# Kernel tuning notes

Measured on AMD Instinct MI355X. Metric: run time of the kernel, lower is better.

## Reference

```python
import jax, jax.numpy as jnp
import numpy as np

HIDDEN = 256
HEADS = 8
DK = HIDDEN // HEADS
BH = 16  # bias_h_size
N = 2048
B = 1


def setup_inputs() -> dict:
    key = jax.random.key(0)
    ks = jax.random.split(key, 20)
    s = 0.02
    inp = {
        "int_chain_label": jax.random.randint(ks[0], (N, N), 0, 2, dtype=jnp.int32),
        "dist_map": jax.random.uniform(ks[1], (N, N), dtype=jnp.float32),
        "contact_map": jax.random.uniform(ks[2], (N, N), dtype=jnp.float32),
        "q": jax.random.normal(ks[3], (B, N, HIDDEN), dtype=jnp.float32),
        "k": jax.random.normal(ks[4], (B, N, HIDDEN), dtype=jnp.float32),
        "v": jax.random.normal(ks[5], (B, N, HIDDEN), dtype=jnp.float32),
        # projections
        "Wq": jax.random.normal(ks[6], (HIDDEN, HIDDEN), dtype=jnp.float32) * s,
        "bq": jnp.zeros((HIDDEN,), jnp.float32),
        "Wk": jax.random.normal(ks[7], (HIDDEN, HIDDEN), dtype=jnp.float32) * s,
        "bk": jnp.zeros((HIDDEN,), jnp.float32),
        "Wv": jax.random.normal(ks[8], (HIDDEN, HIDDEN), dtype=jnp.float32) * s,
        "bv": jnp.zeros((HIDDEN,), jnp.float32),
        "Wo": jax.random.normal(ks[9], (HIDDEN, HIDDEN), dtype=jnp.float32) * s,
        "bo": jnp.zeros((HIDDEN,), jnp.float32),
        # distance bias MLP: Linear(2, BH) -> Linear(BH, 1)
        "Wd1": jax.random.normal(ks[10], (2, BH), dtype=jnp.float32) * 0.5,
        "bd1": jnp.zeros((BH,), jnp.float32),
        "Wd2": jax.random.normal(ks[11], (BH, 1), dtype=jnp.float32) * 0.5,
        "bd2": jnp.zeros((1,), jnp.float32),
        # contact bias MLP
        "Wc1": jax.random.normal(ks[12], (2, BH), dtype=jnp.float32) * 0.5,
        "bc1": jnp.zeros((BH,), jnp.float32),
        "Wc2": jax.random.normal(ks[13], (BH, 1), dtype=jnp.float32) * 0.5,
        "bc2": jnp.zeros((1,), jnp.float32),
    }
    return inp


def _pair_bias(mp, label_f, W1, b1, W2, b2):
    # stack(map, label) -> [N,N,2]; two linears (no nonlinearity in original) -> [N,N]
    x = jnp.stack((mp, label_f), axis=-1)
    h = x @ W1 + b1                      # [N,N,BH]
    return (h @ W2 + b2)[..., 0]          # [N,N]


def reference(int_chain_label, dist_map, contact_map, q, k, v,
              Wq, bq, Wk, bk, Wv, bv, Wo, bo,
              Wd1, bd1, Wd2, bd2, Wc1, bc1, Wc2, bc2):
    label_f = int_chain_label.astype(jnp.float32)
    bias = (_pair_bias(dist_map, label_f, Wd1, bd1, Wd2, bd2)
            + _pair_bias(contact_map, label_f, Wc1, bc1, Wc2, bc2))  # [N,N]
    bias = bias[None, None]  # [1,1,N,N] broadcast over batch, heads

    b, n, _ = q.shape
    scale = DK ** -0.5
    qh = (q @ Wq + bq).reshape(b, n, HEADS, DK).transpose(0, 2, 1, 3) * scale  # [B,H,N,D]
    kh = (k @ Wk + bk).reshape(b, n, HEADS, DK).transpose(0, 2, 1, 3)
    vh = (v @ Wv + bv).reshape(b, n, HEADS, DK).transpose(0, 2, 1, 3)

    scores = jnp.einsum('bhnd,bhmd->bhnm', qh, kh) + bias  # [B,H,N,N]
    attn = jax.nn.softmax(scores, axis=-1)
    out = jnp.einsum('bhnm,bhmd->bhnd', attn, vh)           # [B,H,N,D]
    out = out.transpose(0, 2, 1, 3).reshape(b, n, HEADS * DK)
    return out @ Wo + bo
```

## Files before the change

kernel.cpp:

```cpp
#include <hip/hip_runtime.h>
#include <hip/hip_bf16.h>

#define SN 2048
#define HD 256
#define NHEAD 8
#define DK 32
#define BH 16
#define KCH 4
#define KTILES 8

typedef __bf16 bf16;
typedef __bf16 bf16x8 __attribute__((ext_vector_type(8)));
typedef __bf16 bf16x4 __attribute__((ext_vector_type(4)));
typedef float f32x4 __attribute__((ext_vector_type(4)));
typedef int i32x4 __attribute__((ext_vector_type(4)));

__global__ void __launch_bounds__(256) prep_wt_kernel(
    const float* __restrict__ Wq, const float* __restrict__ Wk,
    const float* __restrict__ Wv, const float* __restrict__ Wo,
    bf16* __restrict__ wt)
{
    __shared__ bf16 tile[32][HD + 8];
    int mat = blockIdx.x >> 3, rc = blockIdx.x & 7;
    int t = threadIdx.x;
    const float* W = mat == 0 ? Wq : mat == 1 ? Wk : mat == 2 ? Wv : Wo;
    bf16* Wt = wt + mat * HD * HD;
    int r0 = rc * 32;
    #pragma unroll
    for (int i = 0; i < 32; i++) tile[i][t] = (bf16)W[(r0 + i) * HD + t];
    __syncthreads();
    #pragma unroll
    for (int i = 0; i < 32; i++) Wt[t * HD + r0 + i] = tile[i][t];
}

template<bool AF32, int MODE, bool OUTF32>
__device__ __forceinline__ void gemm_body(
    const void* __restrict__ Ap, const bf16* __restrict__ Wt,
    const float* __restrict__ bias, void* __restrict__ outp, int bid)
{
    int wave = threadIdx.x >> 6, lane = threadIdx.x & 63;
    int g = lane >> 4, qi = lane & 15;
    int mblk = bid & 31, nblk = bid >> 5;
    int m0 = mblk * 64 + wave * 16, n0 = nblk * 32;
    f32x4 acc0 = {0.f, 0.f, 0.f, 0.f}, acc1 = {0.f, 0.f, 0.f, 0.f};
    const bf16* W0 = Wt + (n0 + qi) * HD + 8 * g;
    const bf16* W1 = W0 + 16 * HD;
    #pragma unroll
    for (int ks = 0; ks < 8; ks++) {
        bf16x8 a;
        if constexpr (AF32) {
            const float* Ar = (const float*)Ap + (m0 + qi) * HD + 8 * g + ks * 32;
            f32x4 lo = *(const f32x4*)Ar;
            f32x4 hi = *(const f32x4*)(Ar + 4);
            #pragma unroll
            for (int e = 0; e < 4; e++) { a[e] = (bf16)lo[e]; a[4 + e] = (bf16)hi[e]; }
        } else {
            a = *(const bf16x8*)((const bf16*)Ap + (m0 + qi) * HD + 8 * g + ks * 32);
        }
        bf16x8 b0 = *(const bf16x8*)(W0 + ks * 32);
        bf16x8 b1 = *(const bf16x8*)(W1 + ks * 32);
        acc0 = __builtin_amdgcn_mfma_f32_16x16x32_bf16(a, b0, acc0, 0, 0, 0);
        acc1 = __builtin_amdgcn_mfma_f32_16x16x32_bf16(a, b1, acc1, 0, 0, 0);
    }
    float bv0 = bias[n0 + qi], bv1 = bias[n0 + 16 + qi];
    if constexpr (MODE == 0) {
        if constexpr (OUTF32) {
            float* out = (float*)outp;
            #pragma unroll
            for (int r = 0; r < 4; r++) {
                int m = m0 + 4 * g + r;
                out[m * HD + n0 + qi]      = acc0[r] + bv0;
                out[m * HD + n0 + 16 + qi] = acc1[r] + bv1;
            }
        } else {
            bf16* out = (bf16*)outp;
            #pragma unroll
            for (int r = 0; r < 4; r++) {
                int m = m0 + 4 * g + r;
                out[m * HD + n0 + qi]      = (bf16)(acc0[r] + bv0);
                out[m * HD + n0 + 16 + qi] = (bf16)(acc1[r] + bv1);
            }
        }
    } else {
        bf16* out = (bf16*)outp;
        bf16x4 v0, v1;
        #pragma unroll
        for (int r = 0; r < 4; r++) { v0[r] = (bf16)(acc0[r] + bv0); v1[r] = (bf16)(acc1[r] + bv1); }
        *(bf16x4*)(out + (n0 + qi) * SN + m0 + 4 * g)      = v0;
        *(bf16x4*)(out + (n0 + 16 + qi) * SN + m0 + 4 * g) = v1;
    }
}

__global__ void __launch_bounds__(256) qkv_kernel(
    const float* __restrict__ q, const float* __restrict__ k, const float* __restrict__ v,
    const bf16* __restrict__ wt,
    const float* __restrict__ bq, const float* __restrict__ bk, const float* __restrict__ bv,
    bf16* __restrict__ qh, bf16* __restrict__ kh, bf16* __restrict__ vt)
{
    int w = blockIdx.y;
    if (w == 0)      gemm_body<true, 0, false>(q, wt,               bq, qh, blockIdx.x);
    else if (w == 1) gemm_body<true, 0, false>(k, wt + HD * HD,     bk, kh, blockIdx.x);
    else             gemm_body<true, 1, false>(v, wt + 2 * HD * HD, bv, vt, blockIdx.x);
}

__global__ void __launch_bounds__(256) oproj_kernel(
    const bf16* __restrict__ A, const bf16* __restrict__ wt3,
    const float* __restrict__ bo, float* __restrict__ out)
{
    gemm_body<false, 0, true>(A, wt3, bo, out, blockIdx.x);
}

__global__ void __launch_bounds__(128) attn_kernel(
    const bf16* __restrict__ qh, const bf16* __restrict__ kh,
    const bf16* __restrict__ vt,
    const int* __restrict__ label, const float* __restrict__ dist,
    const float* __restrict__ contact,
    const float* __restrict__ Wd1, const float* __restrict__ bd1,
    const float* __restrict__ Wd2, const float* __restrict__ bd2,
    const float* __restrict__ Wc1, const float* __restrict__ bc1,
    const float* __restrict__ Wc2, const float* __restrict__ bc2,
    float* __restrict__ po, float* __restrict__ pm, float* __restrict__ pl)
{
    int wave = threadIdx.x >> 6, lane = threadIdx.x & 63;
    int g = lane >> 4, qi = lane & 15;
    int h = blockIdx.x >> 8, qb = (blockIdx.x >> 2) & 63, c = blockIdx.x & 3;
    int q0 = qb * 32 + wave * 16;
    int kbase = c * (KTILES * 64);

    float ad = 0.f, bld = 0.f, dd = bd2[0];
    #pragma unroll
    for (int j = 0; j < BH; j++) {
        float w2 = Wd2[j];
        ad  += Wd1[j] * w2;
        bld += Wd1[BH + j] * w2;
        dd  += bd1[j] * w2;
    }
    float ac = 0.f, blc = 0.f, dc = bc2[0];
    #pragma unroll
    for (int j = 0; j < BH; j++) {
        float w2 = Wc2[j];
        ac  += Wc1[j] * w2;
        blc += Wc1[BH + j] * w2;
        dc  += bc1[j] * w2;
    }
    float bl = bld + blc, dl = dd + dc;

    __shared__ bf16 plds[2][16][72];
    bf16 (*P)[72] = plds[wave];

    bf16x8 qf = *(const bf16x8*)(qh + (q0 + qi) * HD + h * DK + 8 * g);
    const bf16* kp  = kh + h * DK + 8 * g + kbase * HD;
    const bf16* v0p = vt + (h * DK + qi) * SN + 8 * g + kbase;
    const bf16* v1p = v0p + 16 * SN;
    const float* dp = dist    + (q0 + qi) * SN + 4 * g + kbase;
    const float* cp = contact + (q0 + qi) * SN + 4 * g + kbase;
    const int*   lp = label   + (q0 + qi) * SN + 4 * g + kbase;

    const float scale = 0.17677669529663687f;
    float m = -1e30f, lsum = 0.f;
    f32x4 o0 = {0.f, 0.f, 0.f, 0.f}, o1 = {0.f, 0.f, 0.f, 0.f};

    for (int kt = 0; kt < KTILES; kt++) {
        int key0 = kt * 64;
        bf16x8 kf0 = *(const bf16x8*)(kp + (key0 +  0 + qi) * HD);
        bf16x8 kf1 = *(const bf16x8*)(kp + (key0 + 16 + qi) * HD);
        bf16x8 kf2 = *(const bf16x8*)(kp + (key0 + 32 + qi) * HD);
        bf16x8 kf3 = *(const bf16x8*)(kp + (key0 + 48 + qi) * HD);
        f32x4 dv0 = *(const f32x4*)(dp + key0 +  0), dv1 = *(const f32x4*)(dp + key0 + 16);
        f32x4 dv2 = *(const f32x4*)(dp + key0 + 32), dv3 = *(const f32x4*)(dp + key0 + 48);
        f32x4 cv0 = *(const f32x4*)(cp + key0 +  0), cv1 = *(const f32x4*)(cp + key0 + 16);
        f32x4 cv2 = *(const f32x4*)(cp + key0 + 32), cv3 = *(const f32x4*)(cp + key0 + 48);
        i32x4 lv0 = *(const i32x4*)(lp + key0 +  0), lv1 = *(const i32x4*)(lp + key0 + 16);
        i32x4 lv2 = *(const i32x4*)(lp + key0 + 32), lv3 = *(const i32x4*)(lp + key0 + 48);
        f32x4 zero = {0.f, 0.f, 0.f, 0.f};
        f32x4 s0 = __builtin_amdgcn_mfma_f32_16x16x32_bf16(kf0, qf, zero, 0, 0, 0);
        f32x4 s1 = __builtin_amdgcn_mfma_f32_16x16x32_bf16(kf1, qf, zero, 0, 0, 0);
        f32x4 s2 = __builtin_amdgcn_mfma_f32_16x16x32_bf16(kf2, qf, zero, 0, 0, 0);
        f32x4 s3 = __builtin_amdgcn_mfma_f32_16x16x32_bf16(kf3, qf, zero, 0, 0, 0);
        float x[16];
        #pragma unroll
        for (int r = 0; r < 4; r++) {
            float b0 = ad * dv0[r] + ac * cv0[r] + bl * (float)lv0[r] + dl;
            float b1 = ad * dv1[r] + ac * cv1[r] + bl * (float)lv1[r] + dl;
            float b2 = ad * dv2[r] + ac * cv2[r] + bl * (float)lv2[r] + dl;
            float b3 = ad * dv3[r] + ac * cv3[r] + bl * (float)lv3[r] + dl;
            x[r]      = s0[r] * scale + b0;
            x[4 + r]  = s1[r] * scale + b1;
            x[8 + r]  = s2[r] * scale + b2;
            x[12 + r] = s3[r] * scale + b3;
        }
        float t0 = fmaxf(x[0], x[1]),  t1 = fmaxf(x[2], x[3]);
        float t2 = fmaxf(x[4], x[5]),  t3 = fmaxf(x[6], x[7]);
        float t4 = fmaxf(x[8], x[9]),  t5 = fmaxf(x[10], x[11]);
        float t6 = fmaxf(x[12], x[13]), t7 = fmaxf(x[14], x[15]);
        float tm = fmaxf(fmaxf(fmaxf(t0, t1), fmaxf(t2, t3)),
                         fmaxf(fmaxf(t4, t5), fmaxf(t6, t7)));
        tm = fmaxf(tm, __shfl_xor(tm, 16));
        tm = fmaxf(tm, __shfl_xor(tm, 32));
        float mnew = fmaxf(m, tm);
        float f = __expf(m - mnew);
        float ps = 0.f;
        #pragma unroll
        for (int i = 0; i < 16; i++) { x[i] = __expf(x[i] - mnew); ps += x[i]; }
        ps += __shfl_xor(ps, 16);
        ps += __shfl_xor(ps, 32);
        lsum = lsum * f + ps;
        m = mnew;
        #pragma unroll
        for (int r = 0; r < 4; r++) { o0[r] *= f; o1[r] *= f; }
        #pragma unroll
        for (int s = 0; s < 4; s++) {
            bf16x4 pv;
            #pragma unroll
            for (int r = 0; r < 4; r++) pv[r] = (bf16)x[s * 4 + r];
            *(bf16x4*)(&P[qi][16 * s + 4 * g]) = pv;
        }
        asm volatile("" ::: "memory");
        bf16x4 pa0 = *(const bf16x4*)(&P[qi][8 * g]);
        bf16x4 pa1 = *(const bf16x4*)(&P[qi][8 * g + 4]);
        bf16x4 pa2 = *(const bf16x4*)(&P[qi][32 + 8 * g]);
        bf16x4 pa3 = *(const bf16x4*)(&P[qi][32 + 8 * g + 4]);
        asm volatile("" ::: "memory");
        bf16x8 pb0 = __builtin_shufflevector(pa0, pa1, 0, 1, 2, 3, 4, 5, 6, 7);
        bf16x8 pb1 = __builtin_shufflevector(pa2, pa3, 0, 1, 2, 3, 4, 5, 6, 7);
        bf16x8 va00 = *(const bf16x8*)(v0p + key0);
        bf16x8 va01 = *(const bf16x8*)(v0p + key0 + 32);
        bf16x8 va10 = *(const bf16x8*)(v1p + key0);
        bf16x8 va11 = *(const bf16x8*)(v1p + key0 + 32);
        o0 = __builtin_amdgcn_mfma_f32_16x16x32_bf16(va00, pb0, o0, 0, 0, 0);
        o0 = __builtin_amdgcn_mfma_f32_16x16x32_bf16(va01, pb1, o0, 0, 0, 0);
        o1 = __builtin_amdgcn_mfma_f32_16x16x32_bf16(va10, pb0, o1, 0, 0, 0);
        o1 = __builtin_amdgcn_mfma_f32_16x16x32_bf16(va11, pb1, o1, 0, 0, 0);
    }
    int hq = h * SN + q0 + qi;
    *(f32x4*)(po + (hq * KCH + c) * DK + 4 * g)      = o0;
    *(f32x4*)(po + (hq * KCH + c) * DK + 16 + 4 * g) = o1;
    if (g == 0) { pm[hq * KCH + c] = m; pl[hq * KCH + c] = lsum; }
}

__global__ void __launch_bounds__(256) combine_kernel(
    const float* __restrict__ po, const float* __restrict__ pm,
    const float* __restrict__ pl, bf16* __restrict__ aout)
{
    int idx = blockIdx.x * 256 + threadIdx.x;
    int d = idx & (DK - 1), hq = idx >> 5;
    int h = hq >> 11, qr = hq & (SN - 1);
    f32x4 mv = *(const f32x4*)(pm + hq * KCH);
    f32x4 lv = *(const f32x4*)(pl + hq * KCH);
    float M = fmaxf(fmaxf(mv[0], mv[1]), fmaxf(mv[2], mv[3]));
    float w0 = __expf(mv[0] - M), w1 = __expf(mv[1] - M);
    float w2 = __expf(mv[2] - M), w3 = __expf(mv[3] - M);
    float L = w0 * lv[0] + w1 * lv[1] + w2 * lv[2] + w3 * lv[3];
    const float* p = po + hq * KCH * DK + d;
    float o = w0 * p[0] + w1 * p[DK] + w2 * p[2 * DK] + w3 * p[3 * DK];
    aout[qr * HD + h * DK + d] = (bf16)(o / L);
}

extern "C" void kernel_launch(void* const* d_in, const int* in_sizes, int n_in,
                              void* d_out, int out_size, void* d_ws, size_t ws_size,
                              hipStream_t stream)
{
    static const int expect[22] = {
        SN * SN, SN * SN, SN * SN,
        SN * HD, SN * HD, SN * HD,
        HD * HD, HD, HD * HD, HD,
        HD * HD, HD, HD * HD, HD,
        2 * BH, BH, BH, 1,
        2 * BH, BH, BH, 1
    };
    if (n_in != 22) return;
    for (int i = 0; i < 22; i++) if (in_sizes[i] != expect[i]) return;

    const int*   label   = (const int*)  d_in[0];
    const float* dist    = (const float*)d_in[1];
    const float* contact = (const float*)d_in[2];
    const float* q  = (const float*)d_in[3];
    const float* k  = (const float*)d_in[4];
    const float* v  = (const float*)d_in[5];
    const float* Wq = (const float*)d_in[6];  const float* bq = (const float*)d_in[7];
    const float* Wk = (const float*)d_in[8];  const float* bk = (const float*)d_in[9];
    const float* Wv = (const float*)d_in[10]; const float* bv = (const float*)d_in[11];
    const float* Wo = (const float*)d_in[12]; const float* bo = (const float*)d_in[13];
    const float* Wd1 = (const float*)d_in[14]; const float* bd1 = (const float*)d_in[15];
    const float* Wd2 = (const float*)d_in[16]; const float* bd2 = (const float*)d_in[17];
    const float* Wc1 = (const float*)d_in[18]; const float* bc1 = (const float*)d_in[19];
    const float* Wc2 = (const float*)d_in[20]; const float* bc2 = (const float*)d_in[21];

    char* ws = (char*)d_ws;
    bf16*  qh   = (bf16*)(ws);
    bf16*  kh   = (bf16*)(ws + (1u << 20));
    bf16*  vt   = (bf16*)(ws + (2u << 20));
    bf16*  aout = (bf16*)(ws + (3u << 20));
    bf16*  wt   = (bf16*)(ws + (4u << 20));
    float* po   = (float*)(ws + (5u << 20));
    float* pm   = (float*)(ws + (13u << 20));
    float* pl   = (float*)(ws + (13u << 20) + (256u << 10));

    prep_wt_kernel<<<dim3(32), 256, 0, stream>>>(Wq, Wk, Wv, Wo, wt);

    qkv_kernel<<<dim3(256, 3), 256, 0, stream>>>(q, k, v, wt, bq, bk, bv, qh, kh, vt);

    attn_kernel<<<dim3(NHEAD * 64 * KCH), 128, 0, stream>>>(
        qh, kh, vt, label, dist, contact,
        Wd1, bd1, Wd2, bd2, Wc1, bc1, Wc2, bc2, po, pm, pl);

    combine_kernel<<<dim3(NHEAD * SN * DK / 256), 256, 0, stream>>>(po, pm, pl, aout);

    oproj_kernel<<<dim3(256), 256, 0, stream>>>(aout, wt + 3 * HD * HD, bo, (float*)d_out);
}
```

Before: 221.2 us.

## Split attention keys eight ways, use shuffles for P, prefetch GEMM operands

Measured after the change: 222.7 us. No clear change (+0.7%).

```diff
diff --git a/kernel.cpp b/kernel.cpp
--- a/kernel.cpp
+++ b/kernel.cpp
@@ -6,14 +6,13 @@
 #define NHEAD 8
 #define DK 32
 #define BH 16
-#define KCH 4
-#define KTILES 8
 
 typedef __bf16 bf16;
 typedef __bf16 bf16x8 __attribute__((ext_vector_type(8)));
 typedef __bf16 bf16x4 __attribute__((ext_vector_type(4)));
 typedef float f32x4 __attribute__((ext_vector_type(4)));
 typedef int i32x4 __attribute__((ext_vector_type(4)));
+typedef unsigned uint4v __attribute__((ext_vector_type(4)));
 
 __global__ void __launch_bounds__(256) prep_wt_kernel(
     const float* __restrict__ Wq, const float* __restrict__ Wk,
@@ -45,22 +44,35 @@
     f32x4 acc0 = {0.f, 0.f, 0.f, 0.f}, acc1 = {0.f, 0.f, 0.f, 0.f};
     const bf16* W0 = Wt + (n0 + qi) * HD + 8 * g;
     const bf16* W1 = W0 + 16 * HD;
-    #pragma unroll
-    for (int ks = 0; ks < 8; ks++) {
-        bf16x8 a;
+
+    auto loadA = [&](int ks) -> bf16x8 {
         if constexpr (AF32) {
             const float* Ar = (const float*)Ap + (m0 + qi) * HD + 8 * g + ks * 32;
             f32x4 lo = *(const f32x4*)Ar;
             f32x4 hi = *(const f32x4*)(Ar + 4);
+            bf16x8 a;
             #pragma unroll
             for (int e = 0; e < 4; e++) { a[e] = (bf16)lo[e]; a[4 + e] = (bf16)hi[e]; }
+            return a;
         } else {
-            a = *(const bf16x8*)((const bf16*)Ap + (m0 + qi) * HD + 8 * g + ks * 32);
+            return *(const bf16x8*)((const bf16*)Ap + (m0 + qi) * HD + 8 * g + ks * 32);
         }
-        bf16x8 b0 = *(const bf16x8*)(W0 + ks * 32);
-        bf16x8 b1 = *(const bf16x8*)(W1 + ks * 32);
-        acc0 = __builtin_amdgcn_mfma_f32_16x16x32_bf16(a, b0, acc0, 0, 0, 0);
-        acc1 = __builtin_amdgcn_mfma_f32_16x16x32_bf16(a, b1, acc1, 0, 0, 0);
+    };
+
+    bf16x8 a_c  = loadA(0);
+    bf16x8 b0_c = *(const bf16x8*)(W0);
+    bf16x8 b1_c = *(const bf16x8*)(W1);
+    #pragma unroll
+    for (int ks = 0; ks < 8; ks++) {
+        bf16x8 a_n, b0_n, b1_n;
+        if (ks < 7) {
+            a_n  = loadA(ks + 1);
+            b0_n = *(const bf16x8*)(W0 + (ks + 1) * 32);
+            b1_n = *(const bf16x8*)(W1 + (ks + 1) * 32);
+        }
+        acc0 = __builtin_amdgcn_mfma_f32_16x16x32_bf16(a_c, b0_c, acc0, 0, 0, 0);
+        acc1 = __builtin_amdgcn_mfma_f32_16x16x32_bf16(a_c, b1_c, acc1, 0, 0, 0);
+        if (ks < 7) { a_c = a_n; b0_c = b0_n; b1_c = b1_n; }
     }
     float bv0 = bias[n0 + qi], bv1 = bias[n0 + 16 + qi];
     if constexpr (MODE == 0) {
@@ -110,6 +122,7 @@
     gemm_body<false, 0, true>(A, wt3, bo, out, blockIdx.x);
 }
 
+template<int KCHT>
 __global__ void __launch_bounds__(128) attn_kernel(
     const bf16* __restrict__ qh, const bf16* __restrict__ kh,
     const bf16* __restrict__ vt,
@@ -121,11 +134,14 @@
     const float* __restrict__ Wc2, const float* __restrict__ bc2,
     float* __restrict__ po, float* __restrict__ pm, float* __restrict__ pl)
 {
+    constexpr int KT = SN / KCHT / 64;
     int wave = threadIdx.x >> 6, lane = threadIdx.x & 63;
     int g = lane >> 4, qi = lane & 15;
-    int h = blockIdx.x >> 8, qb = (blockIdx.x >> 2) & 63, c = blockIdx.x & 3;
+    int h = blockIdx.x / (64 * KCHT);
+    int rem = blockIdx.x % (64 * KCHT);
+    int qb = rem / KCHT, c = rem % KCHT;
     int q0 = qb * 32 + wave * 16;
-    int kbase = c * (KTILES * 64);
+    int kbase = c * (KT * 64);
 
     float ad = 0.f, bld = 0.f, dd = bd2[0];
     #pragma unroll
@@ -144,9 +160,6 @@
         dc  += bc1[j] * w2;
     }
     float bl = bld + blc, dl = dd + dc;
-
-    __shared__ bf16 plds[2][16][72];
-    bf16 (*P)[72] = plds[wave];
 
     bf16x8 qf = *(const bf16x8*)(qh + (q0 + qi) * HD + h * DK + 8 * g);
     const bf16* kp  = kh + h * DK + 8 * g + kbase * HD;
@@ -160,7 +173,12 @@
     float m = -1e30f, lsum = 0.f;
     f32x4 o0 = {0.f, 0.f, 0.f, 0.f}, o1 = {0.f, 0.f, 0.f, 0.f};
 
-    for (int kt = 0; kt < KTILES; kt++) {
+    int src0 = ((lane >> 4) & 1) * 32 + (lane & 15);
+    int src1 = src0 + 16;
+    bool hi = lane >= 32;
+
+    #pragma unroll
+    for (int kt = 0; kt < KT; kt++) {
         int key0 = kt * 64;
         bf16x8 kf0 = *(const bf16x8*)(kp + (key0 +  0 + qi) * HD);
         bf16x8 kf1 = *(const bf16x8*)(kp + (key0 + 16 + qi) * HD);
@@ -172,6 +190,11 @@
         f32x4 cv2 = *(const f32x4*)(cp + key0 + 32), cv3 = *(const f32x4*)(cp + key0 + 48);
         i32x4 lv0 = *(const i32x4*)(lp + key0 +  0), lv1 = *(const i32x4*)(lp + key0 + 16);
         i32x4 lv2 = *(const i32x4*)(lp + key0 + 32), lv3 = *(const i32x4*)(lp + key0 + 48);
+        bf16x8 va00 = *(const bf16x8*)(v0p + key0);
+        bf16x8 va01 = *(const bf16x8*)(v0p + key0 + 32);
+        bf16x8 va10 = *(const bf16x8*)(v1p + key0);
+        bf16x8 va11 = *(const bf16x8*)(v1p + key0 + 32);
+
         f32x4 zero = {0.f, 0.f, 0.f, 0.f};
         f32x4 s0 = __builtin_amdgcn_mfma_f32_16x16x32_bf16(kf0, qf, zero, 0, 0, 0);
         f32x4 s1 = __builtin_amdgcn_mfma_f32_16x16x32_bf16(kf1, qf, zero, 0, 0, 0);
@@ -189,9 +212,9 @@
             x[8 + r]  = s2[r] * scale + b2;
             x[12 + r] = s3[r] * scale + b3;
         }
-        float t0 = fmaxf(x[0], x[1]),  t1 = fmaxf(x[2], x[3]);
-        float t2 = fmaxf(x[4], x[5]),  t3 = fmaxf(x[6], x[7]);
-        float t4 = fmaxf(x[8], x[9]),  t5 = fmaxf(x[10], x[11]);
+        float t0 = fmaxf(x[0], x[1]),   t1 = fmaxf(x[2], x[3]);
+        float t2 = fmaxf(x[4], x[5]),   t3 = fmaxf(x[6], x[7]);
+        float t4 = fmaxf(x[8], x[9]),   t5 = fmaxf(x[10], x[11]);
         float t6 = fmaxf(x[12], x[13]), t7 = fmaxf(x[14], x[15]);
         float tm = fmaxf(fmaxf(fmaxf(t0, t1), fmaxf(t2, t3)),
                          fmaxf(fmaxf(t4, t5), fmaxf(t6, t7)));
@@ -208,36 +231,42 @@
         m = mnew;
         #pragma unroll
         for (int r = 0; r < 4; r++) { o0[r] *= f; o1[r] *= f; }
-        #pragma unroll
-        for (int s = 0; s < 4; s++) {
-            bf16x4 pv;
-            #pragma unroll
-            for (int r = 0; r < 4; r++) pv[r] = (bf16)x[s * 4 + r];
-            *(bf16x4*)(&P[qi][16 * s + 4 * g]) = pv;
-        }
-        asm volatile("" ::: "memory");
-        bf16x4 pa0 = *(const bf16x4*)(&P[qi][8 * g]);
-        bf16x4 pa1 = *(const bf16x4*)(&P[qi][8 * g + 4]);
-        bf16x4 pa2 = *(const bf16x4*)(&P[qi][32 + 8 * g]);
-        bf16x4 pa3 = *(const bf16x4*)(&P[qi][32 + 8 * g + 4]);
-        asm volatile("" ::: "memory");
-        bf16x8 pb0 = __builtin_shufflevector(pa0, pa1, 0, 1, 2, 3, 4, 5, 6, 7);
-        bf16x8 pb1 = __builtin_shufflevector(pa2, pa3, 0, 1, 2, 3, 4, 5, 6, 7);
-        bf16x8 va00 = *(const bf16x8*)(v0p + key0);
-        bf16x8 va01 = *(const bf16x8*)(v0p + key0 + 32);
-        bf16x8 va10 = *(const bf16x8*)(v1p + key0);
-        bf16x8 va11 = *(const bf16x8*)(v1p + key0 + 32);
+
+        auto PK = [](float a, float b) -> int {
+            unsigned short ua = __builtin_bit_cast(unsigned short, (bf16)a);
+            unsigned short ub = __builtin_bit_cast(unsigned short, (bf16)b);
+            return (int)((unsigned)ua | ((unsigned)ub << 16));
+        };
+        int c0 = PK(x[0], x[1]),  c1 = PK(x[2], x[3]);
+        int c2 = PK(x[4], x[5]),  c3 = PK(x[6], x[7]);
+        int c4 = PK(x[8], x[9]),  c5 = PK(x[10], x[11]);
+        int c6 = PK(x[12], x[13]), c7 = PK(x[14], x[15]);
+
+        unsigned a00 = (unsigned)__shfl(c0, src0), a01 = (unsigned)__shfl(c2, src0);
+        unsigned a10 = (unsigned)__shfl(c1, src0), a11 = (unsigned)__shfl(c3, src0);
+        unsigned a20 = (unsigned)__shfl(c0, src1), a21 = (unsigned)__shfl(c2, src1);
+        unsigned a30 = (unsigned)__shfl(c1, src1), a31 = (unsigned)__shfl(c3, src1);
+        unsigned b00 = (unsigned)__shfl(c4, src0), b01 = (unsigned)__shfl(c6, src0);
+        unsigned b10 = (unsigned)__shfl(c5, src0), b11 = (unsigned)__shfl(c7, src0);
+        unsigned b20 = (unsigned)__shfl(c4, src1), b21 = (unsigned)__shfl(c6, src1);
+        unsigned b30 = (unsigned)__shfl(c5, src1), b31 = (unsigned)__shfl(c7, src1);
+        uint4v u0 = { hi ? a01 : a00, hi ? a11 : a10, hi ? a21 : a20, hi ? a31 : a30 };
+        uint4v u1 = { hi ? b01 : b00, hi ? b11 : b10, hi ? b21 : b20, hi ? b31 : b30 };
+        bf16x8 pb0 = __builtin_bit_cast(bf16x8, u0);
+        bf16x8 pb1 = __builtin_bit_cast(bf16x8, u1);
+
         o0 = __builtin_amdgcn_mfma_f32_16x16x32_bf16(va00, pb0, o0, 0, 0, 0);
         o0 = __builtin_amdgcn_mfma_f32_16x16x32_bf16(va01, pb1, o0, 0, 0, 0);
         o1 = __builtin_amdgcn_mfma_f32_16x16x32_bf16(va10, pb0, o1, 0, 0, 0);
         o1 = __builtin_amdgcn_mfma_f32_16x16x32_bf16(va11, pb1, o1, 0, 0, 0);
     }
     int hq = h * SN + q0 + qi;
-    *(f32x4*)(po + (hq * KCH + c) * DK + 4 * g)      = o0;
-    *(f32x4*)(po + (hq * KCH + c) * DK + 16 + 4 * g) = o1;
-    if (g == 0) { pm[hq * KCH + c] = m; pl[hq * KCH + c] = lsum; }
-}
-
+    *(f32x4*)(po + (hq * KCHT + c) * DK + 4 * g)      = o0;
+    *(f32x4*)(po + (hq * KCHT + c) * DK + 16 + 4 * g) = o1;
+    if (g == 0) { pm[hq * KCHT + c] = m; pl[hq * KCHT + c] = lsum; }
+}
+
+template<int KCHT>
 __global__ void __launch_bounds__(256) combine_kernel(
     const float* __restrict__ po, const float* __restrict__ pm,
     const float* __restrict__ pl, bf16* __restrict__ aout)
@@ -245,14 +274,20 @@
     int idx = blockIdx.x * 256 + threadIdx.x;
     int d = idx & (DK - 1), hq = idx >> 5;
     int h = hq >> 11, qr = hq & (SN - 1);
-    f32x4 mv = *(const f32x4*)(pm + hq * KCH);
-    f32x4 lv = *(const f32x4*)(pl + hq * KCH);
-    float M = fmaxf(fmaxf(mv[0], mv[1]), fmaxf(mv[2], mv[3]));
-    float w0 = __expf(mv[0] - M), w1 = __expf(mv[1] - M);
-    float w2 = __expf(mv[2] - M), w3 = __expf(mv[3] - M);
-    float L = w0 * lv[0] + w1 * lv[1] + w2 * lv[2] + w3 * lv[3];
-    const float* p = po + hq * KCH * DK + d;
-    float o = w0 * p[0] + w1 * p[DK] + w2 * p[2 * DK] + w3 * p[3 * DK];
+    float mv[KCHT], lv[KCHT];
+    #pragma unroll
+    for (int c = 0; c < KCHT; c++) { mv[c] = pm[hq * KCHT + c]; lv[c] = pl[hq * KCHT + c]; }
+    float M = mv[0];
+    #pragma unroll
+    for (int c = 1; c < KCHT; c++) M = fmaxf(M, mv[c]);
+    float L = 0.f, o = 0.f;
+    const float* p = po + hq * KCHT * DK + d;
+    #pragma unroll
+    for (int c = 0; c < KCHT; c++) {
+        float w = __expf(mv[c] - M);
+        L += w * lv[c];
+        o += w * p[c * DK];
+    }
     aout[qr * HD + h * DK + d] = (bf16)(o / L);
 }
 
@@ -293,18 +328,26 @@
     bf16*  aout = (bf16*)(ws + (3u << 20));
     bf16*  wt   = (bf16*)(ws + (4u << 20));
     float* po   = (float*)(ws + (5u << 20));
-    float* pm   = (float*)(ws + (13u << 20));
-    float* pl   = (float*)(ws + (13u << 20) + (256u << 10));
 
     prep_wt_kernel<<<dim3(32), 256, 0, stream>>>(Wq, Wk, Wv, Wo, wt);
-
     qkv_kernel<<<dim3(256, 3), 256, 0, stream>>>(q, k, v, wt, bq, bk, bv, qh, kh, vt);
 
-    attn_kernel<<<dim3(NHEAD * 64 * KCH), 128, 0, stream>>>(
-        qh, kh, vt, label, dist, contact,
-        Wd1, bd1, Wd2, bd2, Wc1, bc1, Wc2, bc2, po, pm, pl);
-
-    combine_kernel<<<dim3(NHEAD * SN * DK / 256), 256, 0, stream>>>(po, pm, pl, aout);
+    size_t need8 = (5u << 20) + (size_t)NHEAD * SN * 8 * DK * 4 + 2u * NHEAD * SN * 8 * 4;
+    if (ws_size >= need8 + (1u << 20)) {
+        float* pm = (float*)(ws + (5u << 20) + (size_t)NHEAD * SN * 8 * DK * 4);
+        float* pl = pm + NHEAD * SN * 8;
+        attn_kernel<8><<<dim3(NHEAD * 64 * 8), 128, 0, stream>>>(
+            qh, kh, vt, label, dist, contact,
+            Wd1, bd1, Wd2, bd2, Wc1, bc1, Wc2, bc2, po, pm, pl);
+        combine_kernel<8><<<dim3(NHEAD * SN * DK / 256), 256, 0, stream>>>(po, pm, pl, aout);
+    } else {
+        float* pm = (float*)(ws + (13u << 20));
+        float* pl = pm + NHEAD * SN * 4;
+        attn_kernel<4><<<dim3(NHEAD * 64 * 4), 128, 0, stream>>>(
+            qh, kh, vt, label, dist, contact,
+            Wd1, bd1, Wd2, bd2, Wc1, bc1, Wc2, bc2, po, pm, pl);
+        combine_kernel<4><<<dim3(NHEAD * SN * DK / 256), 256, 0, stream>>>(po, pm, pl, aout);
+    }
 
     oproj_kernel<<<dim3(256), 256, 0, stream>>>(aout, wt + 3 * HD * HD, bo, (float*)d_out);
 }
```
